# Performance work log

Hardware: AMD Instinct MI355X
Metric: run time of the kernel (lower is better)

## Reference

```python
import jax, jax.numpy as jnp
import numpy as np


def setup_inputs() -> dict:
    key = jax.random.key(0)
    ks = jax.random.split(key, 12)
    B, N, Din, D, K = 2, 1024, 64, 64, 24
    s = lambda fan_in: 1.0 / np.sqrt(fan_in)
    return {
        "feature": jax.random.normal(ks[0], (B, N, Din), jnp.float32),
        "xyz": jax.random.normal(ks[1], (B, N, 3), jnp.float32),
        "pw1": jax.random.uniform(ks[2], (Din, D), jnp.float32, -s(Din), s(Din)),
        "pb1": jax.random.uniform(ks[3], (D,), jnp.float32, -s(Din), s(Din)),
        "pw2": jax.random.uniform(ks[4], (D, D), jnp.float32, -s(D), s(D)),
        "pb2": jax.random.uniform(ks[5], (D,), jnp.float32, -s(D), s(D)),
        "rw": jax.random.uniform(ks[6], (3, D * D), jnp.float32, -s(3), s(3)),
        "rb": jax.random.uniform(ks[7], (D * D,), jnp.float32, -s(3), s(3)),
        "sw": jax.random.uniform(ks[8], (D, D), jnp.float32, -s(D), s(D)),
        "sb": jax.random.uniform(ks[9], (D,), jnp.float32, -s(D), s(D)),
        "knn_num": 24,
    }


def reference(feature, xyz, pw1, pb1, pw2, pb2, rw, rb, sw, sb, knn_num):
    B, N, _ = feature.shape
    D = pw2.shape[1]
    K = knn_num
    # KNN over xyz (squared euclidean distances, smallest K)
    sq = jnp.sum(xyz * xyz, axis=-1)  # [B,N]
    d2 = sq[:, :, None] + sq[:, None, :] - 2.0 * jnp.einsum('bnc,bmc->bnm', xyz, xyz)
    _, idx = jax.lax.top_k(-d2, K)  # [B,N,K]
    bidx = jnp.arange(B)[:, None, None]
    rel = xyz[bidx, idx] - xyz[:, :, None, :]  # [B,N,K,3]
    # prefix MLP: relu(Linear -> ReLU -> Linear)
    feat = jax.nn.relu(jax.nn.relu(feature @ pw1 + pb1) @ pw2 + pb2)  # [B,N,D]
    # per-edge weight generation + softmax over (K*D)
    w = (rel @ rw + rb).reshape(B, N, K * D, D)
    w = jax.nn.softmax(w, axis=-2)
    # gather neighbor features and aggregate
    gv = feat[bidx, idx].reshape(B, N, K * D)  # [B,N,K*D]
    out = jnp.einsum('bnm,bnmd->bnd', gv, w)  # [B,N,D]
    out = out @ sw + sb
    return (out, N)
```

## Files before the change

### kernel.cpp

```cpp
#include <hip/hip_runtime.h>
#include <math.h>

#define BB 2
#define NN 1024
#define DD 64
#define KK 24
#define NPTS (BB * NN)

#if __has_builtin(__builtin_amdgcn_exp2f)
#define EXP2(x) __builtin_amdgcn_exp2f(x)
#else
#define EXP2(x) exp2f(x)
#endif

typedef float v2f __attribute__((ext_vector_type(2)));

static __device__ __forceinline__ v2f pk_fma(v2f a, v2f b, v2f c) {
    v2f d;
    asm("v_pk_fma_f32 %0, %1, %2, %3" : "=v"(d) : "v"(a), "v"(b), "v"(c));
    return d;
}
static __device__ __forceinline__ v2f pk_add(v2f a, v2f b) {
    v2f d;
    asm("v_pk_add_f32 %0, %1, %2" : "=v"(d) : "v"(a), "v"(b));
    return d;
}


__global__ __launch_bounds__(256) void prep_mlp_knn_kernel(
    const float* __restrict__ feature, const float* __restrict__ xyz,
    const float* __restrict__ pw1, const float* __restrict__ pb1,
    const float* __restrict__ pw2, const float* __restrict__ pb2,
    const float* __restrict__ rw, const float* __restrict__ rb,
    float* __restrict__ feat, int* __restrict__ idx_out,
    float4* __restrict__ rwP) {
    int bid = blockIdx.x;
    int tid = threadIdx.x;

    if (bid < 512) {
        int r = tid >> 6;
        int d = tid & 63;
        int row = bid * 4 + r;
        __shared__ float s_in[4][64];
        __shared__ float s_h[4][64];
        s_in[r][d] = feature[row * 64 + d];
        __syncthreads();
        float h = pb1[d];
#pragma unroll
        for (int i = 0; i < 64; i++) h = __builtin_fmaf(s_in[r][i], pw1[i * 64 + d], h);
        h = fmaxf(h, 0.f);
        s_h[r][d] = h;
        __syncthreads();
        float f = pb2[d];
#pragma unroll
        for (int i = 0; i < 64; i++) f = __builtin_fmaf(s_h[r][i], pw2[i * 64 + d], f);
        f = fmaxf(f, 0.f);
        feat[row * 64 + d] = f;
    } else if (bid < 528) {
        const float LOG2E = 1.4426950408889634f;
        int t = (bid - 512) * 256 + tid;
        float4 v;
        v.x = rw[t] * LOG2E;
        v.y = rw[4096 + t] * LOG2E;
        v.z = rw[8192 + t] * LOG2E;
        v.w = rb[t] * LOG2E;
        rwP[t] = v;
    } else {
        int w = tid >> 6;
        int lane = tid & 63;
        int pt = (bid - 528) * 4 + w;
        int b = pt >> 10;
        int n = pt & 1023;
        const float* xb = xyz + (size_t)b * NN * 3;
        float xn = xb[n * 3 + 0], yn = xb[n * 3 + 1], zn = xb[n * 3 + 2];
        float sqn = xn * xn + yn * yn + zn * zn;
        float dist[16];
#pragma unroll
        for (int c = 0; c < 16; c++) {
            int m = c * 64 + lane;
            float xm = xb[m * 3 + 0], ym = xb[m * 3 + 1], zm = xb[m * 3 + 2];
            float sqm = xm * xm + ym * ym + zm * zm;
            float dot = xn * xm + yn * ym + zn * zm;
            dist[c] = sqn + sqm - 2.0f * dot;
        }
        for (int r = 0; r < KK; r++) {
            float best = 3.4e38f;
            int bi = 1 << 30;
#pragma unroll
            for (int c = 0; c < 16; c++) {
                if (dist[c] < best) {
                    best = dist[c];
                    bi = c * 64 + lane;
                }
            }
#pragma unroll
            for (int off = 32; off >= 1; off >>= 1) {
                float ob = __shfl_down(best, off);
                int oi = __shfl_down(bi, off);
                if (ob < best || (ob == best && oi < bi)) {
                    best = ob;
                    bi = oi;
                }
            }
            bi = __shfl(bi, 0);
            if ((bi & 63) == lane) dist[bi >> 6] = 3.4e38f;
            if (lane == 0) idx_out[pt * KK + r] = bi;
        }
    }
}

#define GVS 28
__global__ __launch_bounds__(256, 1) void agg_kernel(const float* __restrict__ xyz,
                                                     const float* __restrict__ feat,
                                                     const int* __restrict__ idx,
                                                     const float4* __restrict__ rwP,
                                                     const float* __restrict__ sw,
                                                     const float* __restrict__ sb,
                                                     float* __restrict__ out) {
    int pt = blockIdx.x;
    int b = pt >> 10;
    int n = pt & 1023;
    int tid = threadIdx.x;
    int w = tid >> 6;
    int d = tid & 63;

    __shared__ __align__(8) float s_relT[3][28];
    __shared__ __align__(16) float s_gvt[64][GVS];
    __shared__ float s_red[8][64];
    __shared__ float s_pre[64];

    const float* xb = xyz + (size_t)b * NN * 3;
    if (tid < KK * 3) {
        int k = tid % KK, c = tid / KK;
        int nb = idx[pt * KK + k];
        s_relT[c][k] = xb[nb * 3 + c] - xb[n * 3 + c];
    }
    for (int t = tid; t < KK * 64; t += 256) {
        int k = t >> 6, j = t & 63;
        int nb = idx[pt * KK + k];
        s_gvt[j][k] = feat[((size_t)b * NN + nb) * 64 + j];
    }
    __syncthreads();

    v2f rx[12], ry[12], rz[12];
#pragma unroll
    for (int k = 0; k < 12; k++) {
        rx[k] = *(const v2f*)&s_relT[0][2 * k];
        ry[k] = *(const v2f*)&s_relT[1][2 * k];
        rz[k] = *(const v2f*)&s_relT[2][2 * k];
    }

    v2f l0 = {0.f, 0.f}, l1 = {0.f, 0.f}, a0 = {0.f, 0.f}, a1 = {0.f, 0.f};
    int col0 = (w * 16) * 64 + d;
    float4 rv = rwP[col0];
    for (int jj = 0; jj < 16; jj++) {
        int j = w * 16 + jj;
        float4 rvn = rv;
        if (jj < 15) rvn = rwP[col0 + (jj + 1) * 64];
        v2f R0 = {rv.x, rv.x}, R1 = {rv.y, rv.y}, R2 = {rv.z, rv.z}, RB = {rv.w, rv.w};
        const float4* g4 = (const float4*)(&s_gvt[j][0]);
#pragma unroll
        for (int q = 0; q < 6; q++) {
            float4 g = g4[q];
            v2f ga = {g.x, g.y};
            v2f gb = {g.z, g.w};
            v2f t0 = pk_fma(rx[2 * q], R0, pk_fma(ry[2 * q], R1, pk_fma(rz[2 * q], R2, RB)));
            v2f t1 = pk_fma(rx[2 * q + 1], R0, pk_fma(ry[2 * q + 1], R1, pk_fma(rz[2 * q + 1], R2, RB)));
            v2f e0 = {EXP2(t0.x), EXP2(t0.y)};
            v2f e1 = {EXP2(t1.x), EXP2(t1.y)};
            l0 = pk_add(l0, e0);
            l1 = pk_add(l1, e1);
            a0 = pk_fma(ga, e0, a0);
            a1 = pk_fma(gb, e1, a1);
        }
        rv = rvn;
    }
    s_red[w][d] = l0.x + l0.y + l1.x + l1.y;
    s_red[4 + w][d] = a0.x + a0.y + a1.x + a1.y;
    __syncthreads();
    if (tid < 64) {
        float L = s_red[0][d] + s_red[1][d] + s_red[2][d] + s_red[3][d];
        float A = s_red[4][d] + s_red[5][d] + s_red[6][d] + s_red[7][d];
        s_pre[d] = A / L;
    }
    __syncthreads();
    float part = 0.f;
#pragma unroll
    for (int dd = 0; dd < 16; dd++) {
        int drow = w * 16 + dd;
        part = __builtin_fmaf(s_pre[drow], sw[drow * 64 + d], part);
    }
    s_red[w][d] = part;
    __syncthreads();
    if (tid < 64) {
        float o = s_red[0][d] + s_red[1][d] + s_red[2][d] + s_red[3][d] + sb[d];
        out[(size_t)pt * 64 + d] = o;
    }
    if (pt == 0 && tid == 0) out[(size_t)NPTS * 64] = 1024.0f;
}

extern "C" void kernel_launch(void* const* d_in, const int* in_sizes, int n_in,
                              void* d_out, int out_size, void* d_ws, size_t ws_size,
                              hipStream_t stream) {
    const float* feature = (const float*)d_in[0];
    const float* xyz = (const float*)d_in[1];
    const float* pw1 = (const float*)d_in[2];
    const float* pb1 = (const float*)d_in[3];
    const float* pw2 = (const float*)d_in[4];
    const float* pb2 = (const float*)d_in[5];
    const float* rw = (const float*)d_in[6];
    const float* rb = (const float*)d_in[7];
    const float* sw = (const float*)d_in[8];
    const float* sb = (const float*)d_in[9];
    float* out = (float*)d_out;

    char* ws = (char*)d_ws;
    float* feat = (float*)(ws);
    int* idx = (int*)(ws + 524288);
    float4* rwP = (float4*)(ws + 720896);

    prep_mlp_knn_kernel<<<1040, 256, 0, stream>>>(feature, xyz, pw1, pb1, pw2, pb2,
                                                  rw, rb, feat, idx, rwP);
    agg_kernel<<<NPTS, 256, 0, stream>>>(xyz, feat, idx, rwP, sw, sb, out);
}
```

Measured before the change: 131.7 us.

## Split aggregation work across waves by neighbor subset instead of column subset

```diff
diff --git a/kernel.cpp b/kernel.cpp
--- a/kernel.cpp
+++ b/kernel.cpp
@@ -109,14 +109,13 @@
     }
 }
 
-#define GVS 28
-__global__ __launch_bounds__(256, 1) void agg_kernel(const float* __restrict__ xyz,
-                                                     const float* __restrict__ feat,
-                                                     const int* __restrict__ idx,
-                                                     const float4* __restrict__ rwP,
-                                                     const float* __restrict__ sw,
-                                                     const float* __restrict__ sb,
-                                                     float* __restrict__ out) {
+__global__ __launch_bounds__(256) void agg_kernel(const float* __restrict__ xyz,
+                                                  const float* __restrict__ feat,
+                                                  const int* __restrict__ idx,
+                                                  const float4* __restrict__ rwP,
+                                                  const float* __restrict__ sw,
+                                                  const float* __restrict__ sb,
+                                                  float* __restrict__ out) {
     int pt = blockIdx.x;
     int b = pt >> 10;
     int n = pt & 1023;
@@ -125,7 +124,7 @@
     int d = tid & 63;
 
     __shared__ __align__(8) float s_relT[3][28];
-    __shared__ __align__(16) float s_gvt[64][GVS];
+    __shared__ __align__(16) float s_gvt[4][64][8];
     __shared__ float s_red[8][64];
     __shared__ float s_pre[64];
 
@@ -138,45 +137,50 @@
     for (int t = tid; t < KK * 64; t += 256) {
         int k = t >> 6, j = t & 63;
         int nb = idx[pt * KK + k];
-        s_gvt[j][k] = feat[((size_t)b * NN + nb) * 64 + j];
-    }
-    __syncthreads();
-
-    v2f rx[12], ry[12], rz[12];
-#pragma unroll
-    for (int k = 0; k < 12; k++) {
-        rx[k] = *(const v2f*)&s_relT[0][2 * k];
-        ry[k] = *(const v2f*)&s_relT[1][2 * k];
-        rz[k] = *(const v2f*)&s_relT[2][2 * k];
-    }
-
-    v2f l0 = {0.f, 0.f}, l1 = {0.f, 0.f}, a0 = {0.f, 0.f}, a1 = {0.f, 0.f};
-    int col0 = (w * 16) * 64 + d;
-    float4 rv = rwP[col0];
-    for (int jj = 0; jj < 16; jj++) {
-        int j = w * 16 + jj;
-        float4 rvn = rv;
-        if (jj < 15) rvn = rwP[col0 + (jj + 1) * 64];
-        v2f R0 = {rv.x, rv.x}, R1 = {rv.y, rv.y}, R2 = {rv.z, rv.z}, RB = {rv.w, rv.w};
-        const float4* g4 = (const float4*)(&s_gvt[j][0]);
-#pragma unroll
-        for (int q = 0; q < 6; q++) {
-            float4 g = g4[q];
-            v2f ga = {g.x, g.y};
-            v2f gb = {g.z, g.w};
-            v2f t0 = pk_fma(rx[2 * q], R0, pk_fma(ry[2 * q], R1, pk_fma(rz[2 * q], R2, RB)));
-            v2f t1 = pk_fma(rx[2 * q + 1], R0, pk_fma(ry[2 * q + 1], R1, pk_fma(rz[2 * q + 1], R2, RB)));
-            v2f e0 = {EXP2(t0.x), EXP2(t0.y)};
-            v2f e1 = {EXP2(t1.x), EXP2(t1.y)};
-            l0 = pk_add(l0, e0);
-            l1 = pk_add(l1, e1);
-            a0 = pk_fma(ga, e0, a0);
-            a1 = pk_fma(gb, e1, a1);
-        }
-        rv = rvn;
-    }
-    s_red[w][d] = l0.x + l0.y + l1.x + l1.y;
-    s_red[4 + w][d] = a0.x + a0.y + a1.x + a1.y;
+        s_gvt[k / 6][j][k % 6] = feat[((size_t)b * NN + nb) * 64 + j];
+    }
+    __syncthreads();
+
+    int k0 = 6 * w;
+    v2f rx[3], ry[3], rz[3];
+#pragma unroll
+    for (int p = 0; p < 3; p++) {
+        rx[p] = *(const v2f*)&s_relT[0][k0 + 2 * p];
+        ry[p] = *(const v2f*)&s_relT[1][k0 + 2 * p];
+        rz[p] = *(const v2f*)&s_relT[2][k0 + 2 * p];
+    }
+
+    v2f l0 = {0.f, 0.f}, l1 = {0.f, 0.f}, l2 = {0.f, 0.f};
+    v2f a0 = {0.f, 0.f}, a1 = {0.f, 0.f}, a2 = {0.f, 0.f};
+
+    const float* gw = &s_gvt[w][0][0];
+    float4 rv0 = rwP[0 * 64 + d];
+    float4 rv1 = rwP[1 * 64 + d];
+    for (int j = 0; j < 64; j++) {
+        float4 rvn = rv1;
+        if (j < 62) rvn = rwP[(j + 2) * 64 + d];
+        v2f R0 = {rv0.x, rv0.x}, R1 = {rv0.y, rv0.y}, R2 = {rv0.z, rv0.z}, RB = {rv0.w, rv0.w};
+        float4 gA = *(const float4*)(gw + j * 8);
+        v2f gC = *(const v2f*)(gw + j * 8 + 4);
+        v2f g0 = {gA.x, gA.y};
+        v2f g1 = {gA.z, gA.w};
+        v2f t0 = pk_fma(rx[0], R0, pk_fma(ry[0], R1, pk_fma(rz[0], R2, RB)));
+        v2f t1 = pk_fma(rx[1], R0, pk_fma(ry[1], R1, pk_fma(rz[1], R2, RB)));
+        v2f t2 = pk_fma(rx[2], R0, pk_fma(ry[2], R1, pk_fma(rz[2], R2, RB)));
+        v2f e0 = {EXP2(t0.x), EXP2(t0.y)};
+        v2f e1 = {EXP2(t1.x), EXP2(t1.y)};
+        v2f e2 = {EXP2(t2.x), EXP2(t2.y)};
+        l0 = pk_add(l0, e0);
+        l1 = pk_add(l1, e1);
+        l2 = pk_add(l2, e2);
+        a0 = pk_fma(g0, e0, a0);
+        a1 = pk_fma(g1, e1, a1);
+        a2 = pk_fma(gC, e2, a2);
+        rv0 = rv1;
+        rv1 = rvn;
+    }
+    s_red[w][d] = l0.x + l0.y + l1.x + l1.y + l2.x + l2.y;
+    s_red[4 + w][d] = a0.x + a0.y + a1.x + a1.y + a2.x + a2.y;
     __syncthreads();
     if (tid < 64) {
         float L = s_red[0][d] + s_red[1][d] + s_red[2][d] + s_red[3][d];
```

After: 144.7 us. +9.9%, slower.
